# Performance work log

Measured on AMD Instinct MI355X. Metric: run time of the kernel, lower is better.

## Reference

```python
import jax, jax.numpy as jnp
import numpy as np

HID = 2560
NH, P, N, G, K = 80, 64, 128, 1, 4
INTER = NH * P            # 5120
CONV_DIM = INTER + 2 * G * N  # 5376
PROJ = INTER + CONV_DIM + NH  # 10576
EPS = 1e-5
DT_MIN, DT_MAX = 0.0, 100.0
BATCH = 64


def setup_inputs() -> dict:
    key = jax.random.key(0)
    ks = jax.random.split(key, 11)
    return {
        "input_states": jax.random.normal(ks[0], (BATCH, 1, HID), jnp.float32),
        "conv_state": 0.1 * jax.random.normal(ks[1], (BATCH, CONV_DIM, K), jnp.float32),
        "ssm_state": 0.1 * jax.random.normal(ks[2], (BATCH, NH, P, N), jnp.float32),
        "in_proj_w": jax.random.normal(ks[3], (PROJ, HID), jnp.float32) * (HID ** -0.5),
        "conv_w": jax.random.normal(ks[4], (CONV_DIM, K), jnp.float32) * 0.2,
        "conv_b": jax.random.normal(ks[5], (CONV_DIM,), jnp.float32) * 0.02,
        "dt_bias": jax.random.normal(ks[6], (NH,), jnp.float32) * 0.1,
        "A_log": jnp.log(jnp.arange(1, NH + 1, dtype=jnp.float32)),
        "D": jnp.ones((NH,), jnp.float32),
        "norm_w": jnp.ones((INTER,), jnp.float32),
        "out_proj_w": jax.random.normal(ks[7], (HID, INTER), jnp.float32) * (INTER ** -0.5),
    }


def reference(input_states, conv_state, ssm_state, in_proj_w, conv_w, conv_b,
              dt_bias, A_log, D, norm_w, out_proj_w):
    B = input_states.shape[0]
    # in_proj: (B,1,HID) @ (HID,PROJ) -> (B,1,PROJ); d_mlp == 0 with these dims
    proj = jnp.einsum("bsh,ph->bsp", input_states, in_proj_w)
    gate = proj[..., :INTER]                       # (B,1,INTER)
    hBC = proj[..., INTER:INTER + CONV_DIM]        # (B,1,CONV_DIM)
    dt = proj[..., INTER + CONV_DIM:]              # (B,1,NH)

    # conv cache update: roll left, append current token
    new_conv_state = jnp.concatenate(
        [conv_state[:, :, 1:], hBC[:, 0, :, None]], axis=-1)  # (B,CONV_DIM,K)
    x = jnp.sum(new_conv_state * conv_w[None], axis=-1) + conv_b  # (B,CONV_DIM)
    x = jax.nn.silu(x)

    hs = x[:, :INTER].reshape(B, NH, P)            # (B,NH,P)
    Bm = x[:, INTER:INTER + G * N].reshape(B, G, N)
    Cm = x[:, INTER + G * N:].reshape(B, G, N)
    Bm = jnp.repeat(Bm, NH // G, axis=1)           # (B,NH,N)
    Cm = jnp.repeat(Cm, NH // G, axis=1)           # (B,NH,N)

    # discretization (dt is per-head, broadcast over head_dim as in source)
    dt_sp = jnp.clip(jax.nn.softplus(dt[:, 0, :] + dt_bias), DT_MIN, DT_MAX)  # (B,NH)
    A = -jnp.exp(A_log)                            # (NH,)
    dA = jnp.exp(dt_sp * A)                        # (B,NH)

    dBx = dt_sp[:, :, None, None] * Bm[:, :, None, :] * hs[..., None]  # (B,NH,P,N)
    new_ssm = ssm_state * dA[:, :, None, None] + dBx                   # (B,NH,P,N)

    y = jnp.einsum("bhpn,bhn->bhp", new_ssm, Cm)   # (B,NH,P)
    y = y + hs * D[None, :, None]
    y = y.reshape(B, 1, INTER)

    # gated RMSNorm (fp32 internals)
    yf = y.astype(jnp.float32) * jax.nn.silu(gate.astype(jnp.float32))
    var = jnp.mean(yf * yf, axis=-1, keepdims=True)
    yn = norm_w * (yf * jax.lax.rsqrt(var + EPS)).astype(y.dtype)

    out = jnp.einsum("bsi,hi->bsh", yn, out_proj_w)  # (B,1,HID)
    return out
```

## Files before the change

kernel.cpp:

```cpp
#include <hip/hip_runtime.h>
#include <stdint.h>

#define HID 2560
#define NH 80
#define PDIM 64
#define NDIM 128
#define INTER 5120
#define CONV_DIM 5376
#define PROJ_DIM 10576
#define NBATCH 64
#define EPS_ 1e-5f

typedef short short8 __attribute__((ext_vector_type(8)));
typedef float f32x4 __attribute__((ext_vector_type(4)));

__device__ __forceinline__ unsigned short f2bf(float f){
  unsigned u = __builtin_bit_cast(unsigned, f);
  u += 0x7FFFu + ((u >> 16) & 1u);
  return (unsigned short)(u >> 16);
}
__device__ __forceinline__ float silu_(float x){ return x / (1.f + __expf(-x)); }

__global__ __launch_bounds__(256) void k_dt(const float* __restrict__ X,
                                            const float* __restrict__ W,
                                            float* __restrict__ dt_part,
                                            unsigned short* __restrict__ Xb){
  const int h = blockIdx.x, ks = blockIdx.y;
  const int tid = threadIdx.x, wid = tid >> 6, lane = tid & 63;
  const float* wr = W + (size_t)(INTER + CONV_DIM + h) * HID + ks * 320;
  float w[5];
  #pragma unroll
  for (int i = 0; i < 5; ++i) w[i] = wr[lane + i * 64];
  #pragma unroll
  for (int bi = 0; bi < 16; ++bi){
    const int b = wid * 16 + bi;
    const float* xr = X + (size_t)b * HID + ks * 320;
    float x[5];
    float acc = 0.f;
    #pragma unroll
    for (int i = 0; i < 5; ++i){ x[i] = xr[lane + i * 64]; acc += x[i] * w[i]; }
    if (h == 0){
      #pragma unroll
      for (int i = 0; i < 5; ++i)
        Xb[(size_t)b * HID + ks * 320 + lane + i * 64] = f2bf(x[i]);
    }
    #pragma unroll
    for (int m = 32; m; m >>= 1) acc += __shfl_xor(acc, m);
    if (lane == 0) dt_part[(ks * NBATCH + b) * NH + h] = acc;
  }
}

__global__ __launch_bounds__(512) void k1_proj(const unsigned short* __restrict__ Xb,
                                               const float* __restrict__ W,
                                               float* __restrict__ proj){
  __shared__ float red[8][64][16];
  const int tid = threadIdx.x;
  const int wid = tid >> 6, lane = tid & 63;
  const int lr = lane & 15, lg = lane >> 4;
  const int n0 = blockIdx.x * 16;
  const int kw = wid * 320 + lg * 8;
  const short* a0p = (const short*)Xb + (size_t)lr * HID + kw;
  const short* a1p = a0p + 16 * HID;
  const short* a2p = a0p + 32 * HID;
  const short* a3p = a0p + 48 * HID;
  const float* bp  = W + (size_t)(n0 + lr) * HID + kw;
  f32x4 acc0 = {0,0,0,0}, acc1 = {0,0,0,0}, acc2 = {0,0,0,0}, acc3 = {0,0,0,0};
  #pragma unroll
  for (int s = 0; s < 10; ++s){
    const int k = s * 32;
    short8 a0 = *(const short8*)(a0p + k);
    short8 a1 = *(const short8*)(a1p + k);
    short8 a2 = *(const short8*)(a2p + k);
    short8 a3 = *(const short8*)(a3p + k);
    float4 b0 = *(const float4*)(bp + k);
    float4 b1 = *(const float4*)(bp + k + 4);
    short8 bb;
    bb[0] = (short)f2bf(b0.x); bb[1] = (short)f2bf(b0.y);
    bb[2] = (short)f2bf(b0.z); bb[3] = (short)f2bf(b0.w);
    bb[4] = (short)f2bf(b1.x); bb[5] = (short)f2bf(b1.y);
    bb[6] = (short)f2bf(b1.z); bb[7] = (short)f2bf(b1.w);
    acc0 = __builtin_amdgcn_mfma_f32_16x16x32_bf16(a0, bb, acc0, 0, 0, 0);
    acc1 = __builtin_amdgcn_mfma_f32_16x16x32_bf16(a1, bb, acc1, 0, 0, 0);
    acc2 = __builtin_amdgcn_mfma_f32_16x16x32_bf16(a2, bb, acc2, 0, 0, 0);
    acc3 = __builtin_amdgcn_mfma_f32_16x16x32_bf16(a3, bb, acc3, 0, 0, 0);
  }
  #pragma unroll
  for (int r = 0; r < 4; ++r){
    red[wid][ 0 + lg*4 + r][lr] = acc0[r];
    red[wid][16 + lg*4 + r][lr] = acc1[r];
    red[wid][32 + lg*4 + r][lr] = acc2[r];
    red[wid][48 + lg*4 + r][lr] = acc3[r];
  }
  __syncthreads();
  for (int idx = tid; idx < 1024; idx += 512){
    const int m = idx >> 4, n = idx & 15;
    float s = 0.f;
    #pragma unroll
    for (int w = 0; w < 8; ++w) s += red[w][m][n];
    proj[(size_t)m * PROJ_DIM + n0 + n] = s;
  }
}

__global__ __launch_bounds__(256) void k2a(const float* __restrict__ cs,
                                           const float* __restrict__ cw,
                                           const float* __restrict__ cb,
                                           const float* __restrict__ proj,
                                           const float* __restrict__ dt_part,
                                           const float* __restrict__ dt_bias,
                                           const float* __restrict__ A_log,
                                           float* __restrict__ hs_bc,
                                           float* __restrict__ dt_sp,
                                           float* __restrict__ dAv,
                                           float* __restrict__ s_bc){
  const int b = blockIdx.y;
  const int c0 = blockIdx.x * 384;
  const int tid = threadIdx.x;
  __shared__ float bc[384];
  for (int i = tid; i < 384; i += 256){
    const int c = c0 + i;
    float4 s4 = *(const float4*)(cs + ((size_t)b * CONV_DIM + c) * 4);
    float4 w4 = *(const float4*)(cw + (size_t)c * 4);
    float hbc = proj[(size_t)b * PROJ_DIM + INTER + c];
    float x = s4.y * w4.x + s4.z * w4.y + s4.w * w4.z + hbc * w4.w + cb[c];
    float v = silu_(x);
    hs_bc[(size_t)b * CONV_DIM + c] = v;
    if (blockIdx.x == 13) bc[i] = v;
  }
  if (blockIdx.x == 0 && tid < NH){
    float acc = dt_bias[tid];
    #pragma unroll
    for (int ks = 0; ks < 8; ++ks) acc += dt_part[(ks * NBATCH + b) * NH + tid];
    float sp = acc > 15.f ? acc : log1pf(__expf(acc));
    sp = fminf(fmaxf(sp, 0.f), 100.f);
    dt_sp[b * NH + tid] = sp;
    dAv[b * NH + tid] = __expf(-sp * __expf(A_log[tid]));
  }
  if (blockIdx.x == 13){
    __syncthreads();
    if (tid < 64){
      float p = bc[128 + tid] * bc[256 + tid] + bc[192 + tid] * bc[320 + tid];
      #pragma unroll
      for (int m = 32; m; m >>= 1) p += __shfl_xor(p, m);
      if (tid == 0) s_bc[b] = p;
    }
  }
}

__global__ __launch_bounds__(256) void k2b(const float* __restrict__ ssm,
                                           const float* __restrict__ hs_bc,
                                           const float* __restrict__ proj,
                                           const float* __restrict__ dt_sp,
                                           const float* __restrict__ dAv,
                                           const float* __restrict__ s_bc,
                                           const float* __restrict__ Dp,
                                           const float* __restrict__ norm_w,
                                           unsigned short* __restrict__ yfb,
                                           float* __restrict__ ssq_part){
  const int h = blockIdx.x, b = blockIdx.y;
  const int tid = threadIdx.x;
  const int wid = tid >> 6, lane = tid & 63;
  const int lr = lane & 15, lg = lane >> 4;
  const float dA_s = dAv[b * NH + h];
  const float coef = dt_sp[b * NH + h] * s_bc[b] + Dp[h];
  const float* Cb = hs_bc + (size_t)b * CONV_DIM + INTER + NDIM;
  float4 c0 = *(const float4*)(Cb + lr * 8);
  float4 c1 = *(const float4*)(Cb + lr * 8 + 4);
  const float* srow = ssm + ((size_t)b * NH + h) * PDIM * NDIM;
  float ssq = 0.f;
  __shared__ float ssql[4];
  #pragma unroll
  for (int r = 0; r < 4; ++r){
    const int p = wid * 16 + r * 4 + lg;
    const float* sp_ = srow + (size_t)p * NDIM + lr * 8;
    float4 v0 = *(const float4*)(sp_);
    float4 v1 = *(const float4*)(sp_ + 4);
    float dot = v0.x*c0.x + v0.y*c0.y + v0.z*c0.z + v0.w*c0.w
              + v1.x*c1.x + v1.y*c1.y + v1.z*c1.z + v1.w*c1.w;
    dot += __shfl_xor(dot, 1); dot += __shfl_xor(dot, 2);
    dot += __shfl_xor(dot, 4); dot += __shfl_xor(dot, 8);
    if (lr == 0){
      const int hp = h * PDIM + p;
      float hs = hs_bc[(size_t)b * CONV_DIM + hp];
      float y = dA_s * dot + hs * coef;
      float g = proj[(size_t)b * PROJ_DIM + hp];
      float yf = y * silu_(g) * norm_w[hp];
      yfb[(size_t)b * INTER + hp] = f2bf(yf);
      ssq += yf * yf;
    }
  }
  #pragma unroll
  for (int m = 32; m; m >>= 1) ssq += __shfl_xor(ssq, m);
  if (lane == 0) ssql[wid] = ssq;
  __syncthreads();
  if (tid == 0) ssq_part[b * NH + h] = ssql[0] + ssql[1] + ssql[2] + ssql[3];
}

__global__ __launch_bounds__(512) void k3_out(const unsigned short* __restrict__ Yb,
                                              const float* __restrict__ W,
                                              float* __restrict__ part){
  __shared__ float red[8][64][16];
  const int tid = threadIdx.x;
  const int wid = tid >> 6, lane = tid & 63;
  const int lr = lane & 15, lg = lane >> 4;
  const int n0 = blockIdx.x * 16;
  const int ks = blockIdx.y;
  const int kw = ks * 1280 + wid * 160 + lg * 8;
  const short* a0p = (const short*)Yb + (size_t)lr * INTER + kw;
  const short* a1p = a0p + 16 * INTER;
  const short* a2p = a0p + 32 * INTER;
  const short* a3p = a0p + 48 * INTER;
  const float* bp  = W + (size_t)(n0 + lr) * INTER + kw;
  f32x4 acc0 = {0,0,0,0}, acc1 = {0,0,0,0}, acc2 = {0,0,0,0}, acc3 = {0,0,0,0};
  #pragma unroll
  for (int s = 0; s < 5; ++s){
    const int k = s * 32;
    short8 a0 = *(const short8*)(a0p + k);
    short8 a1 = *(const short8*)(a1p + k);
    short8 a2 = *(const short8*)(a2p + k);
    short8 a3 = *(const short8*)(a3p + k);
    float4 b0 = *(const float4*)(bp + k);
    float4 b1 = *(const float4*)(bp + k + 4);
    short8 bb;
    bb[0] = (short)f2bf(b0.x); bb[1] = (short)f2bf(b0.y);
    bb[2] = (short)f2bf(b0.z); bb[3] = (short)f2bf(b0.w);
    bb[4] = (short)f2bf(b1.x); bb[5] = (short)f2bf(b1.y);
    bb[6] = (short)f2bf(b1.z); bb[7] = (short)f2bf(b1.w);
    acc0 = __builtin_amdgcn_mfma_f32_16x16x32_bf16(a0, bb, acc0, 0, 0, 0);
    acc1 = __builtin_amdgcn_mfma_f32_16x16x32_bf16(a1, bb, acc1, 0, 0, 0);
    acc2 = __builtin_amdgcn_mfma_f32_16x16x32_bf16(a2, bb, acc2, 0, 0, 0);
    acc3 = __builtin_amdgcn_mfma_f32_16x16x32_bf16(a3, bb, acc3, 0, 0, 0);
  }
  #pragma unroll
  for (int r = 0; r < 4; ++r){
    red[wid][ 0 + lg*4 + r][lr] = acc0[r];
    red[wid][16 + lg*4 + r][lr] = acc1[r];
    red[wid][32 + lg*4 + r][lr] = acc2[r];
    red[wid][48 + lg*4 + r][lr] = acc3[r];
  }
  __syncthreads();
  for (int idx = tid; idx < 1024; idx += 512){
    const int m = idx >> 4, n = idx & 15;
    float s = 0.f;
    #pragma unroll
    for (int w = 0; w < 8; ++w) s += red[w][m][n];
    part[((size_t)ks * NBATCH + m) * 2560 + n0 + n] = s;
  }
}

__global__ __launch_bounds__(256) void k4_norm(const float* __restrict__ part,
                                               const float* __restrict__ ssq_part,
                                               float* __restrict__ out){
  const int b = blockIdx.y;
  const int tid = threadIdx.x;
  __shared__ float w4[4];
  __shared__ float sc;
  float v = (tid < NH) ? ssq_part[b * NH + tid] : 0.f;
  #pragma unroll
  for (int m = 32; m; m >>= 1) v += __shfl_xor(v, m);
  const int wid = tid >> 6, lane = tid & 63;
  if (lane == 0) w4[wid] = v;
  __syncthreads();
  if (tid == 0){
    float total = w4[0] + w4[1] + w4[2] + w4[3];
    sc = rsqrtf(total / (float)INTER + EPS_);
  }
  __syncthreads();
  const int j = blockIdx.x * 256 + tid;
  const size_t idx = (size_t)b * 2560 + j;
  const size_t plane = (size_t)NBATCH * 2560;
  float s = part[idx] + part[plane + idx] + part[2*plane + idx] + part[3*plane + idx];
  out[idx] = sc * s;
}

extern "C" void kernel_launch(void* const* d_in, const int* in_sizes, int n_in,
                              void* d_out, int out_size, void* d_ws, size_t ws_size,
                              hipStream_t stream){
  const float* x_in       = (const float*)d_in[0];
  const float* conv_state = (const float*)d_in[1];
  const float* ssm_state  = (const float*)d_in[2];
  const float* in_proj_w  = (const float*)d_in[3];
  const float* conv_w     = (const float*)d_in[4];
  const float* conv_b     = (const float*)d_in[5];
  const float* dt_bias    = (const float*)d_in[6];
  const float* A_log      = (const float*)d_in[7];
  const float* Dp         = (const float*)d_in[8];
  const float* norm_w     = (const float*)d_in[9];
  const float* out_proj_w = (const float*)d_in[10];
  float* out = (float*)d_out;

  char* ws = (char*)d_ws;
  unsigned short* Xb   = (unsigned short*)(ws);
  float* dt_part       = (float*)(ws + 327680);
  float* proj          = (float*)(ws + 491520);
  float* hs_bc         = (float*)(ws + 3198976);
  float* dt_sp         = (float*)(ws + 4575232);
  float* dAv           = (float*)(ws + 4595712);
  float* s_bc          = (float*)(ws + 4616192);
  float* ssq           = (float*)(ws + 4616448);
  unsigned short* Yb   = (unsigned short*)(ws + 4636928);
  float* part          = (float*)(ws + 5292288);

  k_dt<<<dim3(NH, 8), dim3(256), 0, stream>>>(x_in, in_proj_w, dt_part, Xb);
  k1_proj<<<dim3(PROJ_DIM / 16), dim3(512), 0, stream>>>(Xb, in_proj_w, proj);
  k2a<<<dim3(14, NBATCH), dim3(256), 0, stream>>>(conv_state, conv_w, conv_b, proj,
                                                  dt_part, dt_bias, A_log,
                                                  hs_bc, dt_sp, dAv, s_bc);
  k2b<<<dim3(NH, NBATCH), dim3(256), 0, stream>>>(ssm_state, hs_bc, proj, dt_sp, dAv,
                                                  s_bc, Dp, norm_w, Yb, ssq);
  k3_out<<<dim3(160, 4), dim3(512), 0, stream>>>(Yb, out_proj_w, part);
  k4_norm<<<dim3(10, NBATCH), dim3(256), 0, stream>>>(part, ssq, out);
}
```

Before: 137.8 us.

## Use single-wave blocks with full-K loops in projection GEMMs, drop LDS reduction

Both MFMA GEMM kernels (in_proj and out_proj) move from 512-thread blocks that split K across 8 waves and reduce through shared memory to one-wave blocks. Each wave now loops over the whole K range (80 or 40 steps, unrolled by 4) and writes its accumulators straight to global memory. This removes the LDS traffic and the block barrier, but it cuts the number of waves in flight by a factor of eight. These GEMMs are memory-bound weight streams, so per-wave serial latency could limit bandwidth.

```diff
diff --git a/kernel.cpp b/kernel.cpp
--- a/kernel.cpp
+++ b/kernel.cpp
@@ -50,28 +50,22 @@
   }
 }
 
-__global__ __launch_bounds__(512) void k1_proj(const unsigned short* __restrict__ Xb,
-                                               const float* __restrict__ W,
-                                               float* __restrict__ proj){
-  __shared__ float red[8][64][16];
-  const int tid = threadIdx.x;
-  const int wid = tid >> 6, lane = tid & 63;
+__global__ __launch_bounds__(64) void k1_proj(const unsigned short* __restrict__ Xb,
+                                              const float* __restrict__ W,
+                                              float* __restrict__ proj){
+  const int lane = threadIdx.x;
   const int lr = lane & 15, lg = lane >> 4;
   const int n0 = blockIdx.x * 16;
-  const int kw = wid * 320 + lg * 8;
-  const short* a0p = (const short*)Xb + (size_t)lr * HID + kw;
-  const short* a1p = a0p + 16 * HID;
-  const short* a2p = a0p + 32 * HID;
-  const short* a3p = a0p + 48 * HID;
-  const float* bp  = W + (size_t)(n0 + lr) * HID + kw;
+  const short* ap = (const short*)Xb + (size_t)lr * HID + lg * 8;
+  const float* bp = W + (size_t)(n0 + lr) * HID + lg * 8;
   f32x4 acc0 = {0,0,0,0}, acc1 = {0,0,0,0}, acc2 = {0,0,0,0}, acc3 = {0,0,0,0};
-  #pragma unroll
-  for (int s = 0; s < 10; ++s){
+  #pragma unroll 4
+  for (int s = 0; s < 80; ++s){
     const int k = s * 32;
-    short8 a0 = *(const short8*)(a0p + k);
-    short8 a1 = *(const short8*)(a1p + k);
-    short8 a2 = *(const short8*)(a2p + k);
-    short8 a3 = *(const short8*)(a3p + k);
+    short8 a0 = *(const short8*)(ap + k);
+    short8 a1 = *(const short8*)(ap + 16 * HID + k);
+    short8 a2 = *(const short8*)(ap + 32 * HID + k);
+    short8 a3 = *(const short8*)(ap + 48 * HID + k);
     float4 b0 = *(const float4*)(bp + k);
     float4 b1 = *(const float4*)(bp + k + 4);
     short8 bb;
@@ -86,18 +80,11 @@
   }
   #pragma unroll
   for (int r = 0; r < 4; ++r){
-    red[wid][ 0 + lg*4 + r][lr] = acc0[r];
-    red[wid][16 + lg*4 + r][lr] = acc1[r];
-    red[wid][32 + lg*4 + r][lr] = acc2[r];
-    red[wid][48 + lg*4 + r][lr] = acc3[r];
-  }
-  __syncthreads();
-  for (int idx = tid; idx < 1024; idx += 512){
-    const int m = idx >> 4, n = idx & 15;
-    float s = 0.f;
-    #pragma unroll
-    for (int w = 0; w < 8; ++w) s += red[w][m][n];
-    proj[(size_t)m * PROJ_DIM + n0 + n] = s;
+    const int m = lg * 4 + r;
+    proj[(size_t)(m     ) * PROJ_DIM + n0 + lr] = acc0[r];
+    proj[(size_t)(m + 16) * PROJ_DIM + n0 + lr] = acc1[r];
+    proj[(size_t)(m + 32) * PROJ_DIM + n0 + lr] = acc2[r];
+    proj[(size_t)(m + 48) * PROJ_DIM + n0 + lr] = acc3[r];
   }
 }
 
@@ -195,29 +182,24 @@
   if (tid == 0) ssq_part[b * NH + h] = ssql[0] + ssql[1] + ssql[2] + ssql[3];
 }
 
-__global__ __launch_bounds__(512) void k3_out(const unsigned short* __restrict__ Yb,
-                                              const float* __restrict__ W,
-                                              float* __restrict__ part){
-  __shared__ float red[8][64][16];
-  const int tid = threadIdx.x;
-  const int wid = tid >> 6, lane = tid & 63;
+__global__ __launch_bounds__(64) void k3_out(const unsigned short* __restrict__ Yb,
+                                             const float* __restrict__ W,
+                                             float* __restrict__ part){
+  const int lane = threadIdx.x;
   const int lr = lane & 15, lg = lane >> 4;
   const int n0 = blockIdx.x * 16;
   const int ks = blockIdx.y;
-  const int kw = ks * 1280 + wid * 160 + lg * 8;
-  const short* a0p = (const short*)Yb + (size_t)lr * INTER + kw;
-  const short* a1p = a0p + 16 * INTER;
-  const short* a2p = a0p + 32 * INTER;
-  const short* a3p = a0p + 48 * INTER;
-  const float* bp  = W + (size_t)(n0 + lr) * INTER + kw;
+  const int kb = ks * 1280;
+  const short* ap = (const short*)Yb + (size_t)lr * INTER + kb + lg * 8;
+  const float* bp = W + (size_t)(n0 + lr) * INTER + kb + lg * 8;
   f32x4 acc0 = {0,0,0,0}, acc1 = {0,0,0,0}, acc2 = {0,0,0,0}, acc3 = {0,0,0,0};
-  #pragma unroll
-  for (int s = 0; s < 5; ++s){
+  #pragma unroll 4
+  for (int s = 0; s < 40; ++s){
     const int k = s * 32;
-    short8 a0 = *(const short8*)(a0p + k);
-    short8 a1 = *(const short8*)(a1p + k);
-    short8 a2 = *(const short8*)(a2p + k);
-    short8 a3 = *(const short8*)(a3p + k);
+    short8 a0 = *(const short8*)(ap + k);
+    short8 a1 = *(const short8*)(ap + 16 * INTER + k);
+    short8 a2 = *(const short8*)(ap + 32 * INTER + k);
+    short8 a3 = *(const short8*)(ap + 48 * INTER + k);
     float4 b0 = *(const float4*)(bp + k);
     float4 b1 = *(const float4*)(bp + k + 4);
     short8 bb;
@@ -230,20 +212,14 @@
     acc2 = __builtin_amdgcn_mfma_f32_16x16x32_bf16(a2, bb, acc2, 0, 0, 0);
     acc3 = __builtin_amdgcn_mfma_f32_16x16x32_bf16(a3, bb, acc3, 0, 0, 0);
   }
+  float* pt = part + (size_t)ks * NBATCH * 2560;
   #pragma unroll
   for (int r = 0; r < 4; ++r){
-    red[wid][ 0 + lg*4 + r][lr] = acc0[r];
-    red[wid][16 + lg*4 + r][lr] = acc1[r];
-    red[wid][32 + lg*4 + r][lr] = acc2[r];
-    red[wid][48 + lg*4 + r][lr] = acc3[r];
-  }
-  __syncthreads();
-  for (int idx = tid; idx < 1024; idx += 512){
-    const int m = idx >> 4, n = idx & 15;
-    float s = 0.f;
-    #pragma unroll
-    for (int w = 0; w < 8; ++w) s += red[w][m][n];
-    part[((size_t)ks * NBATCH + m) * 2560 + n0 + n] = s;
+    const int m = lg * 4 + r;
+    pt[(size_t)(m     ) * 2560 + n0 + lr] = acc0[r];
+    pt[(size_t)(m + 16) * 2560 + n0 + lr] = acc1[r];
+    pt[(size_t)(m + 32) * 2560 + n0 + lr] = acc2[r];
+    pt[(size_t)(m + 48) * 2560 + n0 + lr] = acc3[r];
   }
 }
 
@@ -301,12 +277,12 @@
   float* part          = (float*)(ws + 5292288);
 
   k_dt<<<dim3(NH, 8), dim3(256), 0, stream>>>(x_in, in_proj_w, dt_part, Xb);
-  k1_proj<<<dim3(PROJ_DIM / 16), dim3(512), 0, stream>>>(Xb, in_proj_w, proj);
+  k1_proj<<<dim3(PROJ_DIM / 16), dim3(64), 0, stream>>>(Xb, in_proj_w, proj);
   k2a<<<dim3(14, NBATCH), dim3(256), 0, stream>>>(conv_state, conv_w, conv_b, proj,
                                                   dt_part, dt_bias, A_log,
                                                   hs_bc, dt_sp, dAv, s_bc);
   k2b<<<dim3(NH, NBATCH), dim3(256), 0, stream>>>(ssm_state, hs_bc, proj, dt_sp, dAv,
                                                   s_bc, Dp, norm_w, Yb, ssq);
-  k3_out<<<dim3(160, 4), dim3(512), 0, stream>>>(Yb, out_proj_w, part);
+  k3_out<<<dim3(160, 4), dim3(64), 0, stream>>>(Yb, out_proj_w, part);
   k4_norm<<<dim3(10, NBATCH), dim3(256), 0, stream>>>(part, ssq, out);
 }
```

New measurement: 136.5 us. No clear change (-1.0%).
